# Kernel tuning notes

Hardware: AMD Instinct MI355X
Metric: run time of the kernel (lower is better)

Reference implementation:

```python
import jax, jax.numpy as jnp
import numpy as np

B = 1; H = 256; W = 256; C = 192; HEADS = 6; WS = 16; SHIFT = 8
N = WS * WS; HD = C // HEADS; HID = 4 * C


def setup_inputs() -> dict:
    key = jax.random.key(0)
    ks = jax.random.split(key, 8)
    # relative position index (standard Swin construction)
    coords = np.stack(np.meshgrid(np.arange(WS), np.arange(WS), indexing='ij'))  # 2,ws,ws
    cf = coords.reshape(2, -1)
    rel = (cf[:, :, None] - cf[:, None, :]).transpose(1, 2, 0)  # n,n,2
    rel[..., 0] += WS - 1
    rel[..., 1] += WS - 1
    rel[..., 0] *= 2 * WS - 1
    rpi = rel.sum(-1).astype(np.int32)  # [N,N], values in [0, (2*WS-1)^2)
    # shifted-window attention mask (standard Swin construction)
    img = np.zeros((1, H, W, 1), np.float32)
    cnt = 0
    sl = (slice(0, -WS), slice(-WS, -SHIFT), slice(-SHIFT, None))
    for hs in sl:
        for ws_ in sl:
            img[:, hs, ws_, :] = cnt
            cnt += 1
    mw = img.reshape(1, H // WS, WS, W // WS, WS, 1).transpose(0, 1, 3, 2, 4, 5).reshape(-1, N)
    diff = mw[:, None, :] - mw[:, :, None]  # [nw, N, N]
    attn_mask = np.where(diff != 0, np.float32(-100.0), np.float32(0.0))
    std = 0.02
    p = lambda k, shp: jax.random.normal(k, shp, jnp.float32) * std
    return {
        'x': jax.random.normal(ks[0], (B, H * W, C), jnp.float32),
        'rpi_sa': jnp.asarray(rpi),
        'attn_mask': jnp.asarray(attn_mask),
        'norm1_g': jnp.ones((C,), jnp.float32), 'norm1_b': jnp.zeros((C,), jnp.float32),
        'qkv_w': p(ks[1], (C, 3 * C)), 'qkv_b': jnp.zeros((3 * C,), jnp.float32),
        'rpb_table': p(ks[2], ((2 * WS - 1) * (2 * WS - 1), HEADS)),
        'proj_w': p(ks[3], (C, C)), 'proj_b': jnp.zeros((C,), jnp.float32),
        'norm2_g': jnp.ones((C,), jnp.float32), 'norm2_b': jnp.zeros((C,), jnp.float32),
        'fc1_w': p(ks[4], (C, HID)), 'fc1_b': jnp.zeros((HID,), jnp.float32),
        'fc2_w': p(ks[5], (HID, C)), 'fc2_b': jnp.zeros((C,), jnp.float32),
    }


def _ln(x, g, b):
    m = x.mean(-1, keepdims=True)
    v = ((x - m) ** 2).mean(-1, keepdims=True)
    return (x - m) * jax.lax.rsqrt(v + 1e-5) * g + b


def reference(x, rpi_sa, attn_mask, norm1_g, norm1_b, qkv_w, qkv_b, rpb_table,
              proj_w, proj_b, norm2_g, norm2_b, fc1_w, fc1_b, fc2_w, fc2_b):
    b = x.shape[0]
    shortcut = x
    h = _ln(x, norm1_g, norm1_b).reshape(b, H, W, C)
    h = jnp.roll(h, (-SHIFT, -SHIFT), axis=(1, 2))
    # window partition -> (b*nw, N, C)
    xw = h.reshape(b, H // WS, WS, W // WS, WS, C).transpose(0, 1, 3, 2, 4, 5).reshape(-1, N, C)
    qkv = (xw @ qkv_w + qkv_b).reshape(-1, N, 3, HEADS, HD).transpose(2, 0, 3, 1, 4)
    q, k, v = qkv[0] * (HD ** -0.5), qkv[1], qkv[2]  # [b_, H, N, HD]
    attn = jnp.einsum('bhnd,bhmd->bhnm', q, k)  # [b_, H, N, N]
    bias = rpb_table[rpi_sa.reshape(-1)].reshape(N, N, HEADS).transpose(2, 0, 1)
    attn = attn + bias[None]
    nw = attn_mask.shape[0]
    attn = attn.reshape(-1, nw, HEADS, N, N) + attn_mask[None, :, None]
    attn = jax.nn.softmax(attn.reshape(-1, HEADS, N, N), axis=-1)
    out = jnp.einsum('bhnm,bhmd->bnhd', attn, v).reshape(-1, N, C)
    out = out @ proj_w + proj_b
    # window reverse + unshift
    out = out.reshape(b, H // WS, W // WS, WS, WS, C).transpose(0, 1, 3, 2, 4, 5).reshape(b, H, W, C)
    out = jnp.roll(out, (SHIFT, SHIFT), axis=(1, 2)).reshape(b, H * W, C)
    xr = shortcut + out  # drop_path = identity (eval / drop_prob=0)
    y = _ln(xr, norm2_g, norm2_b)
    y = jax.nn.gelu(y @ fc1_w + fc1_b, approximate=False) @ fc2_w + fc2_b
    return xr + y
```

## Files before the change

kernel.cpp:

```cpp
#include <hip/hip_runtime.h>
#include <math.h>

#define NHEADS 6
#define CC 192
#define HDIM 32
#define NTOK 256
#define SHIFTV 8

typedef __attribute__((ext_vector_type(8))) short short8;
typedef __attribute__((ext_vector_type(4))) short short4v;
typedef __attribute__((ext_vector_type(4))) float floatx4;

__device__ inline short f2bf(float f) {
    union { float f; unsigned u; } v; v.f = f;
    unsigned r = (v.u + 0x7FFFu + ((v.u >> 16) & 1u)) >> 16;
    return (short)r;
}

__device__ inline float gelu_f(float x) {
    float x2 = x * x;
    float p = x * (-1.5957691216f - 0.07135481627f * x2);
    float e = __expf(p);
    return x * __builtin_amdgcn_rcpf(1.f + e);
}

__global__ __launch_bounds__(256) void bias_kernel(const int* __restrict__ rpi,
                                                   const float* __restrict__ rpb,
                                                   float* __restrict__ biasB) {
    int idx = blockIdx.x * 256 + threadIdx.x;
    int m = idx & 255;
    int n = (idx >> 8) & 255;
    int h = idx >> 16;
    biasB[idx] = rpb[rpi[n * 256 + m] * NHEADS + h];
}

__global__ __launch_bounds__(256) void cvt_kernel(const float* __restrict__ qkvw,
                                                  const float* __restrict__ pw,
                                                  const float* __restrict__ f1w,
                                                  const float* __restrict__ f2w,
                                                  short* __restrict__ wqt,
                                                  short* __restrict__ pwt,
                                                  short* __restrict__ w1t,
                                                  short* __restrict__ w2t) {
    int idx = blockIdx.x * 256 + threadIdx.x;
    int n = idx / 192, k = idx - n * 192;
    w1t[idx] = f2bf(f1w[k * 768 + n]);
    int c = idx / 768, h = idx - c * 768;
    w2t[idx] = f2bf(f2w[h * 192 + c]);
    if (idx < 576 * 192) wqt[idx] = f2bf(qkvw[k * 576 + n]);
    if (idx < 192 * 192) pwt[idx] = f2bf(pw[k * 192 + n]);
}

__global__ __launch_bounds__(256) void qkv_kernel(const float* __restrict__ x,
        const float* __restrict__ g1, const float* __restrict__ b1,
        const short* __restrict__ wqt, const float* __restrict__ qkvb,
        ushort* __restrict__ Qb, ushort* __restrict__ Kb, ushort* __restrict__ VTb) {
    __shared__ __align__(16) short xln[64 * 200];
    __shared__ float red[64][4][2];
    const int t = threadIdx.x;
    const int g0 = blockIdx.x * 64;
    const int w = g0 >> 8;
    {
        int row = t >> 2, part = t & 3;
        int n = (g0 + row) & 255;
        int sy = (((w >> 4) << 4) + (n >> 4) + SHIFTV) & 255;
        int sx = (((w & 15) << 4) + (n & 15) + SHIFTV) & 255;
        const float* xr = x + (sy * 256 + sx) * CC + part * 48;
        float vals[48];
        float s = 0.f, ss = 0.f;
        #pragma unroll
        for (int i = 0; i < 48; ++i) { float v = xr[i]; vals[i] = v; s += v; ss += v * v; }
        red[row][part][0] = s; red[row][part][1] = ss;
        __syncthreads();
        float sum = red[row][0][0] + red[row][1][0] + red[row][2][0] + red[row][3][0];
        float sq  = red[row][0][1] + red[row][1][1] + red[row][2][1] + red[row][3][1];
        float mean = sum * (1.f / 192.f);
        float var = sq * (1.f / 192.f) - mean * mean;
        float inv = rsqrtf(var + 1e-5f);
        #pragma unroll
        for (int i = 0; i < 48; ++i) {
            int c = part * 48 + i;
            xln[row * 200 + c] = f2bf((vals[i] - mean) * inv * g1[c] + b1[c]);
        }
    }
    __syncthreads();
    const int wv = t >> 6, lane = t & 63;
    const int lr = lane & 15;
    const int lk = (lane >> 4) * 8;
    const int q4 = (lane >> 4) * 4;
    #pragma unroll
    for (int jc = 0; jc < 3; ++jc) {
        floatx4 acc[4][3];
        #pragma unroll
        for (int mt = 0; mt < 4; ++mt)
            #pragma unroll
            for (int nt = 0; nt < 3; ++nt) acc[mt][nt] = floatx4{0.f,0.f,0.f,0.f};
        for (int ks = 0; ks < 6; ++ks) {
            int k0 = ks * 32 + lk;
            short8 a[4];
            #pragma unroll
            for (int mt = 0; mt < 4; ++mt)
                a[mt] = *(const short8*)&xln[(mt * 16 + lr) * 200 + k0];
            #pragma unroll
            for (int nt = 0; nt < 3; ++nt) {
                int nglob = jc * 192 + wv * 48 + nt * 16 + lr;
                short8 b = *(const short8*)&wqt[nglob * 192 + k0];
                #pragma unroll
                for (int mt = 0; mt < 4; ++mt)
                    acc[mt][nt] = __builtin_amdgcn_mfma_f32_16x16x32_bf16(a[mt], b, acc[mt][nt], 0, 0, 0);
            }
        }
        #pragma unroll
        for (int nt = 0; nt < 3; ++nt) {
            int jj = wv * 48 + nt * 16 + lr;
            float bias = qkvb[jc * 192 + jj];
            int head = jj >> 5, hd = jj & 31;
            int wh = w * NHEADS + head;
            #pragma unroll
            for (int mt = 0; mt < 4; ++mt) {
                int nr0 = (g0 + mt * 16 + q4) & 255;
                if (jc == 0) {
                    #pragma unroll
                    for (int reg = 0; reg < 4; ++reg)
                        Qb[((size_t)wh * NTOK + nr0 + reg) * HDIM + hd] =
                            (ushort)f2bf((acc[mt][nt][reg] + bias) * 0.17677669529663687f);
                } else if (jc == 1) {
                    #pragma unroll
                    for (int reg = 0; reg < 4; ++reg)
                        Kb[((size_t)wh * NTOK + nr0 + reg) * HDIM + hd] =
                            (ushort)f2bf(acc[mt][nt][reg] + bias);
                } else {
                    short4v pk;
                    #pragma unroll
                    for (int reg = 0; reg < 4; ++reg)
                        pk[reg] = f2bf(acc[mt][nt][reg] + bias);
                    *(short4v*)&VTb[((size_t)wh * HDIM + hd) * NTOK + nr0] = pk;
                }
            }
        }
    }
}

__global__ __launch_bounds__(256) void attn_kernel(const ushort* __restrict__ Q,
        const ushort* __restrict__ K, const ushort* __restrict__ VT,
        const float* __restrict__ biasB, const float* __restrict__ mask,
        ushort* __restrict__ Ob) {
    __shared__ __align__(16) ushort Ks[256 * 40];
    __shared__ __align__(16) ushort Vs[32 * 264];
    __shared__ __align__(16) ushort Ps[4][64 * 40];
    const int t = threadIdx.x;
    const int wh = blockIdx.x;
    const int w = wh / 6, h = wh - w * 6;
    {
        const ushort* kg = K + (size_t)wh * (NTOK * HDIM);
        const ushort* vg = VT + (size_t)wh * (NTOK * HDIM);
        for (int i = t * 8; i < NTOK * HDIM; i += 2048) {
            short8 kv = *(const short8*)(kg + i);
            *(short8*)&Ks[(i >> 5) * 40 + (i & 31)] = kv;
            short8 vv = *(const short8*)(vg + i);
            *(short8*)&Vs[(i >> 8) * 264 + (i & 255)] = vv;
        }
    }
    const int wv = t >> 6, lane = t & 63;
    const int lc = lane & 15;
    const int q4 = (lane >> 4) * 4;
    const int lk8 = (lane >> 4) * 8;
    const int qb = wv * 64;
    short8 qf[4];
    {
        const ushort* qg = Q + (size_t)wh * (NTOK * HDIM);
        #pragma unroll
        for (int qt = 0; qt < 4; ++qt)
            qf[qt] = *(const short8*)(qg + (qb + qt * 16 + lc) * HDIM + lk8);
    }
    __syncthreads();
    float Ssum[4];
    floatx4 o[2][4];
    #pragma unroll
    for (int qt = 0; qt < 4; ++qt) {
        Ssum[qt] = 0.f;
        o[0][qt] = floatx4{0.f,0.f,0.f,0.f};
        o[1][qt] = floatx4{0.f,0.f,0.f,0.f};
    }
    ushort* Pw = &Ps[wv][0];
    const float* bp = biasB + h * 65536;
    const float* mp = mask + (size_t)w * 65536;
    for (int kc = 0; kc < 8; ++kc) {
        const int k0 = kc * 32;
        short8 ka[2];
        ka[0] = *(const short8*)&Ks[(k0 + lc) * 40 + lk8];
        ka[1] = *(const short8*)&Ks[(k0 + 16 + lc) * 40 + lk8];
        floatx4 sf[2][4];
        #pragma unroll
        for (int kt = 0; kt < 2; ++kt)
            #pragma unroll
            for (int qt = 0; qt < 4; ++qt)
                sf[kt][qt] = __builtin_amdgcn_mfma_f32_16x16x32_bf16(ka[kt], qf[qt],
                                floatx4{0.f,0.f,0.f,0.f}, 0, 0, 0);
        #pragma unroll
        for (int kt = 0; kt < 2; ++kt)
            #pragma unroll
            for (int qt = 0; qt < 4; ++qt) {
                int q = qb + qt * 16 + lc;
                int kbase = k0 + kt * 16 + q4;
                float4 bb = *(const float4*)(bp + q * 256 + kbase);
                float4 mm = *(const float4*)(mp + q * 256 + kbase);
                float p0 = __expf(sf[kt][qt][0] + bb.x + mm.x);
                float p1 = __expf(sf[kt][qt][1] + bb.y + mm.y);
                float p2 = __expf(sf[kt][qt][2] + bb.z + mm.z);
                float p3 = __expf(sf[kt][qt][3] + bb.w + mm.w);
                Ssum[qt] += (p0 + p1) + (p2 + p3);
                short4v pk;
                pk.x = f2bf(p0); pk.y = f2bf(p1); pk.z = f2bf(p2); pk.w = f2bf(p3);
                *(short4v*)&Pw[(qt * 16 + lc) * 40 + kt * 16 + q4] = pk;
            }
        short8 va[2], pf[4];
        va[0] = *(const short8*)&Vs[lc * 264 + k0 + lk8];
        va[1] = *(const short8*)&Vs[(16 + lc) * 264 + k0 + lk8];
        #pragma unroll
        for (int qt = 0; qt < 4; ++qt)
            pf[qt] = *(const short8*)&Pw[(qt * 16 + lc) * 40 + lk8];
        #pragma unroll
        for (int ht = 0; ht < 2; ++ht)
            #pragma unroll
            for (int qt = 0; qt < 4; ++qt)
                o[ht][qt] = __builtin_amdgcn_mfma_f32_16x16x32_bf16(va[ht], pf[qt], o[ht][qt], 0, 0, 0);
    }
    #pragma unroll
    for (int qt = 0; qt < 4; ++qt) {
        float rs = Ssum[qt];
        rs += __shfl_xor(rs, 16);
        rs += __shfl_xor(rs, 32);
        float inv = 1.f / rs;
        size_t rowbase = ((size_t)(w * NTOK + qb + qt * 16 + lc)) * CC + h * HDIM;
        #pragma unroll
        for (int ht = 0; ht < 2; ++ht)
            #pragma unroll
            for (int r = 0; r < 4; ++r)
                Ob[rowbase + ht * 16 + q4 + r] = (ushort)f2bf(o[ht][qt][r] * inv);
    }
}

__global__ __launch_bounds__(256) void proj_kernel(const ushort* __restrict__ Ob,
        const short* __restrict__ pwt, const float* __restrict__ pb,
        const float* __restrict__ x, float* __restrict__ out) {
    __shared__ __align__(16) short oln[64 * 200];
    const int t = threadIdx.x;
    const int g0 = blockIdx.x * 64;
    const int w = g0 >> 8;
    {
        int row = t >> 2, part = t & 3;
        const ushort* orow = Ob + (size_t)(g0 + row) * CC + part * 48;
        #pragma unroll
        for (int i = 0; i < 6; ++i)
            *(short8*)&oln[row * 200 + part * 48 + i * 8] = *(const short8*)(orow + i * 8);
    }
    __syncthreads();
    const int wv = t >> 6, lane = t & 63;
    const int lr = lane & 15;
    const int lk = (lane >> 4) * 8;
    const int q4 = (lane >> 4) * 4;
    floatx4 acc[4][3];
    #pragma unroll
    for (int mt = 0; mt < 4; ++mt)
        #pragma unroll
        for (int nt = 0; nt < 3; ++nt) acc[mt][nt] = floatx4{0.f,0.f,0.f,0.f};
    for (int ks = 0; ks < 6; ++ks) {
        int k0 = ks * 32 + lk;
        short8 a[4];
        #pragma unroll
        for (int mt = 0; mt < 4; ++mt)
            a[mt] = *(const short8*)&oln[(mt * 16 + lr) * 200 + k0];
        #pragma unroll
        for (int nt = 0; nt < 3; ++nt) {
            int c = wv * 48 + nt * 16 + lr;
            short8 b = *(const short8*)&pwt[c * 192 + k0];
            #pragma unroll
            for (int mt = 0; mt < 4; ++mt)
                acc[mt][nt] = __builtin_amdgcn_mfma_f32_16x16x32_bf16(a[mt], b, acc[mt][nt], 0, 0, 0);
        }
    }
    #pragma unroll
    for (int nt = 0; nt < 3; ++nt) {
        int c = wv * 48 + nt * 16 + lr;
        float bias = pb[c];
        #pragma unroll
        for (int mt = 0; mt < 4; ++mt) {
            #pragma unroll
            for (int reg = 0; reg < 4; ++reg) {
                int nn = (g0 + mt * 16 + q4 + reg) & 255;
                int sy = (((w >> 4) << 4) + (nn >> 4) + SHIFTV) & 255;
                int sx = (((w & 15) << 4) + (nn & 15) + SHIFTV) & 255;
                size_t base = (size_t)(sy * 256 + sx) * CC;
                out[base + c] = x[base + c] + acc[mt][nt][reg] + bias;
            }
        }
    }
}

__global__ __launch_bounds__(256) void mlp_kernel(const float* __restrict__ g2,
        const float* __restrict__ b2, const short* __restrict__ w1t,
        const float* __restrict__ f1b, const short* __restrict__ w2t,
        const float* __restrict__ f2b, float* __restrict__ out) {
    __shared__ __align__(16) short xln[64 * 200];
    __shared__ __align__(16) short Hs[64 * 200];
    __shared__ float red[64][4][2];
    const int t = threadIdx.x;
    const int m0 = blockIdx.x * 64;
    {
        int row = t >> 2, part = t & 3;
        const float* xr = out + (size_t)(m0 + row) * CC + part * 48;
        float vals[48];
        float s = 0.f, ss = 0.f;
        #pragma unroll
        for (int i = 0; i < 48; ++i) { float v = xr[i]; vals[i] = v; s += v; ss += v * v; }
        red[row][part][0] = s; red[row][part][1] = ss;
        __syncthreads();
        float sum = red[row][0][0] + red[row][1][0] + red[row][2][0] + red[row][3][0];
        float sq  = red[row][0][1] + red[row][1][1] + red[row][2][1] + red[row][3][1];
        float mean = sum * (1.f / 192.f);
        float var = sq * (1.f / 192.f) - mean * mean;
        float inv = rsqrtf(var + 1e-5f);
        #pragma unroll
        for (int i = 0; i < 48; ++i) {
            int c = part * 48 + i;
            xln[row * 200 + c] = f2bf((vals[i] - mean) * inv * g2[c] + b2[c]);
        }
    }
    __syncthreads();
    const int wv = t >> 6;
    const int lane = t & 63;
    const int lr = lane & 15;
    const int lk = (lane >> 4) * 8;
    const int q4 = (lane >> 4) * 4;
    floatx4 acc2[4][3];
    #pragma unroll
    for (int mt = 0; mt < 4; ++mt)
        #pragma unroll
        for (int nt = 0; nt < 3; ++nt) acc2[mt][nt] = floatx4{0.f, 0.f, 0.f, 0.f};

    for (int hc = 0; hc < 4; ++hc) {
        floatx4 acc1[4][3];
        #pragma unroll
        for (int mt = 0; mt < 4; ++mt)
            #pragma unroll
            for (int nt = 0; nt < 3; ++nt) acc1[mt][nt] = floatx4{0.f, 0.f, 0.f, 0.f};
        for (int ks = 0; ks < 6; ++ks) {
            int k0 = ks * 32 + lk;
            short8 a[4];
            #pragma unroll
            for (int mt = 0; mt < 4; ++mt)
                a[mt] = *(const short8*)&xln[(mt * 16 + lr) * 200 + k0];
            #pragma unroll
            for (int nt = 0; nt < 3; ++nt) {
                int n = hc * 192 + wv * 48 + nt * 16 + lr;
                short8 b = *(const short8*)&w1t[n * 192 + k0];
                #pragma unroll
                for (int mt = 0; mt < 4; ++mt)
                    acc1[mt][nt] = __builtin_amdgcn_mfma_f32_16x16x32_bf16(a[mt], b, acc1[mt][nt], 0, 0, 0);
            }
        }
        __syncthreads();
        #pragma unroll
        for (int nt = 0; nt < 3; ++nt) {
            int colb = wv * 48 + nt * 16 + lr;
            float bias = f1b[hc * 192 + colb];
            #pragma unroll
            for (int mt = 0; mt < 4; ++mt) {
                #pragma unroll
                for (int reg = 0; reg < 4; ++reg) {
                    float v = acc1[mt][nt][reg] + bias;
                    Hs[(mt * 16 + q4 + reg) * 200 + colb] = f2bf(gelu_f(v));
                }
            }
        }
        __syncthreads();
        for (int ks = 0; ks < 6; ++ks) {
            int k0 = ks * 32 + lk;
            short8 a[4];
            #pragma unroll
            for (int mt = 0; mt < 4; ++mt)
                a[mt] = *(const short8*)&Hs[(mt * 16 + lr) * 200 + k0];
            #pragma unroll
            for (int nt = 0; nt < 3; ++nt) {
                int c = wv * 48 + nt * 16 + lr;
                short8 b = *(const short8*)&w2t[c * 768 + hc * 192 + k0];
                #pragma unroll
                for (int mt = 0; mt < 4; ++mt)
                    acc2[mt][nt] = __builtin_amdgcn_mfma_f32_16x16x32_bf16(a[mt], b, acc2[mt][nt], 0, 0, 0);
            }
        }
    }
    #pragma unroll
    for (int nt = 0; nt < 3; ++nt) {
        int c = wv * 48 + nt * 16 + lr;
        float bias = f2b[c];
        #pragma unroll
        for (int mt = 0; mt < 4; ++mt) {
            #pragma unroll
            for (int reg = 0; reg < 4; ++reg) {
                size_t off = (size_t)(m0 + mt * 16 + q4 + reg) * CC + c;
                out[off] = out[off] + acc2[mt][nt][reg] + bias;
            }
        }
    }
}

extern "C" void kernel_launch(void* const* d_in, const int* in_sizes, int n_in,
                              void* d_out, int out_size, void* d_ws, size_t ws_size,
                              hipStream_t stream) {
    (void)in_sizes; (void)n_in; (void)out_size; (void)ws_size;
    const float* x    = (const float*)d_in[0];
    const int*   rpi  = (const int*)d_in[1];
    const float* mask = (const float*)d_in[2];
    const float* n1g  = (const float*)d_in[3];
    const float* n1b  = (const float*)d_in[4];
    const float* qkvw = (const float*)d_in[5];
    const float* qkvb = (const float*)d_in[6];
    const float* rpb  = (const float*)d_in[7];
    const float* pw   = (const float*)d_in[8];
    const float* pb   = (const float*)d_in[9];
    const float* n2g  = (const float*)d_in[10];
    const float* n2b  = (const float*)d_in[11];
    const float* f1w  = (const float*)d_in[12];
    const float* f1b  = (const float*)d_in[13];
    const float* f2w  = (const float*)d_in[14];
    const float* f2b  = (const float*)d_in[15];
    float* out = (float*)d_out;

    ushort* Qb  = (ushort*)d_ws;
    ushort* Kb  = Qb + 12582912;
    ushort* VTb = Kb + 12582912;
    ushort* Ob  = VTb + 12582912;
    float* BIAS = (float*)(Ob + 12582912);
    short* WQT  = (short*)(BIAS + 393216);
    short* PWT  = WQT + 110592;
    short* W1T  = PWT + 36864;
    short* W2T  = W1T + 147456;

    bias_kernel<<<1536, 256, 0, stream>>>(rpi, rpb, BIAS);
    cvt_kernel<<<576, 256, 0, stream>>>(qkvw, pw, f1w, f2w, WQT, PWT, W1T, W2T);
    qkv_kernel<<<1024, 256, 0, stream>>>(x, n1g, n1b, WQT, qkvb, Qb, Kb, VTb);
    attn_kernel<<<1536, 256, 0, stream>>>(Qb, Kb, VTb, BIAS, mask, Ob);
    proj_kernel<<<1024, 256, 0, stream>>>(Ob, PWT, pb, x, out);
    mlp_kernel<<<1024, 256, 0, stream>>>(n2g, n2b, W1T, f1b, W2T, f2b, out);
}
```

Measured before the change: 484.3 us.

## Give each MLP wave its own 16-row slice to drop block-wide barriers

The MLP kernel previously split the 64-row tile across the four waves by output column, so every stage needed a block-wide __syncthreads. Now each wave owns 16 rows end to end and computes all 192 hidden/output columns for them. LayerNorm reductions use warp shuffles, and the per-wave LDS buffers remove every barrier. In exchange, each wave reloads the full w1t/w2t weights from global memory (four times the weight traffic per block), and A-operand reuse per B load drops from 4 to 1.

```diff
diff --git a/kernel.cpp b/kernel.cpp
--- a/kernel.cpp
+++ b/kernel.cpp
@@ -302,106 +302,89 @@
         const float* __restrict__ b2, const short* __restrict__ w1t,
         const float* __restrict__ f1b, const short* __restrict__ w2t,
         const float* __restrict__ f2b, float* __restrict__ out) {
-    __shared__ __align__(16) short xln[64 * 200];
-    __shared__ __align__(16) short Hs[64 * 200];
-    __shared__ float red[64][4][2];
+    __shared__ __align__(16) short xln[4][16 * 200];
+    __shared__ __align__(16) short Hs[4][16 * 200];
     const int t = threadIdx.x;
-    const int m0 = blockIdx.x * 64;
-    {
-        int row = t >> 2, part = t & 3;
-        const float* xr = out + (size_t)(m0 + row) * CC + part * 48;
-        float vals[48];
-        float s = 0.f, ss = 0.f;
-        #pragma unroll
-        for (int i = 0; i < 48; ++i) { float v = xr[i]; vals[i] = v; s += v; ss += v * v; }
-        red[row][part][0] = s; red[row][part][1] = ss;
-        __syncthreads();
-        float sum = red[row][0][0] + red[row][1][0] + red[row][2][0] + red[row][3][0];
-        float sq  = red[row][0][1] + red[row][1][1] + red[row][2][1] + red[row][3][1];
-        float mean = sum * (1.f / 192.f);
-        float var = sq * (1.f / 192.f) - mean * mean;
-        float inv = rsqrtf(var + 1e-5f);
-        #pragma unroll
-        for (int i = 0; i < 48; ++i) {
-            int c = part * 48 + i;
-            xln[row * 200 + c] = f2bf((vals[i] - mean) * inv * g2[c] + b2[c]);
-        }
-    }
-    __syncthreads();
-    const int wv = t >> 6;
-    const int lane = t & 63;
+    const int wv = t >> 6, lane = t & 63;
     const int lr = lane & 15;
     const int lk = (lane >> 4) * 8;
     const int q4 = (lane >> 4) * 4;
-    floatx4 acc2[4][3];
-    #pragma unroll
-    for (int mt = 0; mt < 4; ++mt)
-        #pragma unroll
-        for (int nt = 0; nt < 3; ++nt) acc2[mt][nt] = floatx4{0.f, 0.f, 0.f, 0.f};
+    const int m0 = blockIdx.x * 64 + wv * 16;
+    short* xw = &xln[wv][0];
+    short* hw = &Hs[wv][0];
+    {
+        int part = lane >> 4;
+        const float* xr = out + (size_t)(m0 + lr) * CC + part * 48;
+        float vals[48];
+        float s = 0.f, ss = 0.f;
+        #pragma unroll
+        for (int i = 0; i < 48; ++i) { float v = xr[i]; vals[i] = v; s += v; ss += v * v; }
+        s += __shfl_xor(s, 16);  ss += __shfl_xor(ss, 16);
+        s += __shfl_xor(s, 32);  ss += __shfl_xor(ss, 32);
+        float mean = s * (1.f / 192.f);
+        float var = ss * (1.f / 192.f) - mean * mean;
+        float inv = rsqrtf(var + 1e-5f);
+        #pragma unroll
+        for (int i = 0; i < 48; ++i) {
+            int c = part * 48 + i;
+            xw[lr * 200 + c] = f2bf((vals[i] - mean) * inv * g2[c] + b2[c]);
+        }
+    }
+    floatx4 acc2[12];
+    #pragma unroll
+    for (int nt = 0; nt < 12; ++nt) acc2[nt] = floatx4{0.f, 0.f, 0.f, 0.f};
 
     for (int hc = 0; hc < 4; ++hc) {
-        floatx4 acc1[4][3];
-        #pragma unroll
-        for (int mt = 0; mt < 4; ++mt)
-            #pragma unroll
-            for (int nt = 0; nt < 3; ++nt) acc1[mt][nt] = floatx4{0.f, 0.f, 0.f, 0.f};
+        floatx4 acc1[12];
+        #pragma unroll
+        for (int nt = 0; nt < 12; ++nt) acc1[nt] = floatx4{0.f, 0.f, 0.f, 0.f};
         for (int ks = 0; ks < 6; ++ks) {
             int k0 = ks * 32 + lk;
-            short8 a[4];
-            #pragma unroll
-            for (int mt = 0; mt < 4; ++mt)
-                a[mt] = *(const short8*)&xln[(mt * 16 + lr) * 200 + k0];
-            #pragma unroll
-            for (int nt = 0; nt < 3; ++nt) {
-                int n = hc * 192 + wv * 48 + nt * 16 + lr;
-                short8 b = *(const short8*)&w1t[n * 192 + k0];
+            short8 a = *(const short8*)&xw[lr * 200 + k0];
+            #pragma unroll
+            for (int ng = 0; ng < 3; ++ng) {
                 #pragma unroll
-                for (int mt = 0; mt < 4; ++mt)
-                    acc1[mt][nt] = __builtin_amdgcn_mfma_f32_16x16x32_bf16(a[mt], b, acc1[mt][nt], 0, 0, 0);
-            }
-        }
-        __syncthreads();
-        #pragma unroll
-        for (int nt = 0; nt < 3; ++nt) {
-            int colb = wv * 48 + nt * 16 + lr;
+                for (int nj = 0; nj < 4; ++nj) {
+                    int nt = ng * 4 + nj;
+                    int n = hc * 192 + nt * 16 + lr;
+                    short8 b = *(const short8*)&w1t[n * 192 + k0];
+                    acc1[nt] = __builtin_amdgcn_mfma_f32_16x16x32_bf16(a, b, acc1[nt], 0, 0, 0);
+                }
+            }
+        }
+        #pragma unroll
+        for (int nt = 0; nt < 12; ++nt) {
+            int colb = nt * 16 + lr;
             float bias = f1b[hc * 192 + colb];
             #pragma unroll
-            for (int mt = 0; mt < 4; ++mt) {
-                #pragma unroll
-                for (int reg = 0; reg < 4; ++reg) {
-                    float v = acc1[mt][nt][reg] + bias;
-                    Hs[(mt * 16 + q4 + reg) * 200 + colb] = f2bf(gelu_f(v));
-                }
-            }
-        }
-        __syncthreads();
+            for (int reg = 0; reg < 4; ++reg) {
+                float v = acc1[nt][reg] + bias;
+                hw[(q4 + reg) * 200 + colb] = f2bf(gelu_f(v));
+            }
+        }
         for (int ks = 0; ks < 6; ++ks) {
             int k0 = ks * 32 + lk;
-            short8 a[4];
-            #pragma unroll
-            for (int mt = 0; mt < 4; ++mt)
-                a[mt] = *(const short8*)&Hs[(mt * 16 + lr) * 200 + k0];
-            #pragma unroll
-            for (int nt = 0; nt < 3; ++nt) {
-                int c = wv * 48 + nt * 16 + lr;
-                short8 b = *(const short8*)&w2t[c * 768 + hc * 192 + k0];
+            short8 a = *(const short8*)&hw[lr * 200 + k0];
+            #pragma unroll
+            for (int ng = 0; ng < 3; ++ng) {
                 #pragma unroll
-                for (int mt = 0; mt < 4; ++mt)
-                    acc2[mt][nt] = __builtin_amdgcn_mfma_f32_16x16x32_bf16(a[mt], b, acc2[mt][nt], 0, 0, 0);
-            }
-        }
-    }
-    #pragma unroll
-    for (int nt = 0; nt < 3; ++nt) {
-        int c = wv * 48 + nt * 16 + lr;
+                for (int nj = 0; nj < 4; ++nj) {
+                    int nt = ng * 4 + nj;
+                    int c = nt * 16 + lr;
+                    short8 b = *(const short8*)&w2t[c * 768 + hc * 192 + k0];
+                    acc2[nt] = __builtin_amdgcn_mfma_f32_16x16x32_bf16(a, b, acc2[nt], 0, 0, 0);
+                }
+            }
+        }
+    }
+    #pragma unroll
+    for (int nt = 0; nt < 12; ++nt) {
+        int c = nt * 16 + lr;
         float bias = f2b[c];
         #pragma unroll
-        for (int mt = 0; mt < 4; ++mt) {
-            #pragma unroll
-            for (int reg = 0; reg < 4; ++reg) {
-                size_t off = (size_t)(m0 + mt * 16 + q4 + reg) * CC + c;
-                out[off] = out[off] + acc2[mt][nt][reg] + bias;
-            }
+        for (int reg = 0; reg < 4; ++reg) {
+            size_t off = (size_t)(m0 + q4 + reg) * CC + c;
+            out[off] = out[off] + acc2[nt][reg] + bias;
         }
     }
 }
```

After: 795.1 us. 1.64x slower.
